# Performance work log

Hardware: AMD Instinct MI355X
Metric: run time of the kernel (lower is better)

The kernel has to match this reference:

```python
import jax, jax.numpy as jnp
import numpy as np

T = 8192  # number of points; covariance is T x T


def _rbf_cov(T_, lengthscale, variance):
    # Vectorized replacement of the O(T^2) python-loop kernel evaluation:
    # k(i, j) = variance * exp(-(i - j)^2 / (2 * lengthscale^2)) over integer grid.
    idx = jnp.arange(T_, dtype=jnp.float32)
    d = idx[:, None] - idx[None, :]                      # [T, T]
    return variance * jnp.exp(-(d * d) / (2.0 * lengthscale * lengthscale))


def setup_inputs() -> dict:
    key = jax.random.key(0)
    k1, = jax.random.split(key, 1)
    y = jax.random.normal(k1, (T,), dtype=jnp.float32)
    sigma_sq = jnp.ones((1,), dtype=jnp.float32)
    lengthscale = jnp.asarray(32.0, dtype=jnp.float32)
    variance = jnp.asarray(1.0, dtype=jnp.float32)
    return {"y": y, "sigma_sq": sigma_sq, "lengthscale": lengthscale, "variance": variance}


def reference(y, sigma_sq, lengthscale, variance):
    T_ = y.shape[0]
    K = _rbf_cov(T_, lengthscale, variance)              # [T, T]
    A = K + sigma_sq[0] * jnp.eye(T_, dtype=K.dtype)     # K + sigma^2 I
    yc = y.reshape(T_, 1)
    Ainv = jnp.linalg.inv(A)
    quad = yc.T @ Ainv @ yc                              # [1, 1]
    _, logdet = jnp.linalg.slogdet(A)
    return -0.5 * quad - 0.5 * logdet                    # [1, 1]
```

## Files before the change

### kernel.cpp

```cpp
#include <hip/hip_runtime.h>
#include <math.h>

#define T_PTS 8192
#define NSOLVE 64
#define NLOG   64
#define NBLK   (NSOLVE + NLOG + 1)
#define NTHR   512
#define NWAVE  (NTHR / 64)
#define NPT    128
#define PPT    10
#define WIN    (NPT * PPT)
#define CH     (T_PTS / NSOLVE)
#define HALO   ((WIN - CH) / 2)
#define BS     144
#define NGQ    3
#define NSTEP  3
#define GL     144
#define LDSN   1580
#define JH     256
#define BF     256
#define JB     (T_PTS / NLOG)
#define TQ     (BF / 4)
#define KCORR  768
#define MAGIC  0x13579BDFu

struct Slot { double q, l0, l1; unsigned int flag, pad; };

__device__ inline double blockReduceSum(double v, double* lds) {
#pragma unroll
    for (int o = 32; o > 0; o >>= 1) v += __shfl_down(v, o, 64);
    const int lane = threadIdx.x & 63, wid = threadIdx.x >> 6;
    __syncthreads();
    if (lane == 0) lds[wid] = v;
    __syncthreads();
    double r = 0.0;
    if (threadIdx.x == 0) {
#pragma unroll
        for (int i = 0; i < NWAVE; ++i) r += lds[i];
    }
    return r;
}

struct SolverSh {
    float dbuf[2][LDSN];
    float pac[3][PPT][NPT];
    float wAt[BS];
    float gt[BS];
    float hj[JH];
    float hpart[2][JH];
    float gpart[2][BS + 1];
    float gcen;
};
struct LogdetSh {
    float lgl[JB];
    float wlg[BF + 1];
    float pfj[4][JB];
};
union ShMem { SolverSh s; LogdetSh l; };

__global__ __launch_bounds__(NTHR, 1) void gp_mll_kernel(
    const float* __restrict__ y, const float* __restrict__ s2p,
    const float* __restrict__ ellp, const float* __restrict__ varp,
    float* __restrict__ out, unsigned char* __restrict__ wsb)
{
    __shared__ __align__(16) ShMem sh;
    __shared__ double redd[NWAVE];

    Slot*  slots = (Slot*)wsb;
    float* ckp   = (float*)(wsb + 4096);

    const int tid = threadIdx.x, bid = blockIdx.x;
    const float sig2 = s2p[0], ell = ellp[0], var = varp[0];
    const float inv2l2 = 1.0f / (2.0f * ell * ell);
    const float ang0 = 7.66990393942820614859e-4f;

    if (bid < NSOLVE) {
        SolverSh& S = sh.s;
        for (int d = tid; d < BS; d += NTHR)
            S.wAt[d] = var * expf(-(float)((d + 1) * (d + 1)) * inv2l2);
        for (int i = tid; i < LDSN; i += NTHR) { S.dbuf[0][i] = 0.f; S.dbuf[1][i] = 0.f; }
        __syncthreads();
        const float acen = sig2 + var;

        {
            const int jj = tid & 255, half = tid >> 8;
            float pf = (half == 0) ? acen : 0.f;
            for (int i = 0; i < BS / 2; ++i) {
                const int d = half * (BS / 2) + 1 + i;
                int m = (jj * d) & (T_PTS - 1);
                if (m >= T_PTS / 2) m -= T_PTS;
                pf += 2.f * S.wAt[d - 1] * __cosf(ang0 * (float)m);
            }
            S.hpart[half][jj] = pf;
        }
        __syncthreads();
        if (tid < JH) {
            const float fj = S.hpart[0][tid] + S.hpart[1][tid];
            S.hj[tid] = (fj - sig2) / fj;
        }
        __syncthreads();
        {
            const int d = tid & 255, jh = tid >> 8;
            if (d <= BS) {
                float pg = (jh == 0) ? S.hj[0] : 0.f;
                const int j0 = jh ? 128 : 1, j1 = jh ? 256 : 128;
                for (int j = j0; j < j1; ++j) {
                    int m = (j * d) & (T_PTS - 1);
                    if (m >= T_PTS / 2) m -= T_PTS;
                    pg += 2.f * S.hj[j] * __cosf(ang0 * (float)m);
                }
                S.gpart[jh][d] = pg;
            }
        }
        __syncthreads();
        if (tid <= BS) {
            const float hd = (S.gpart[0][tid] + S.gpart[1][tid]) * (1.0f / (float)T_PTS);
            if (tid == 0) S.gcen = (1.f - hd) / sig2;
            else          S.gt[tid - 1] = -hd / sig2;
        }

        const int pt = tid & (NPT - 1);
        const int q  = tid >> 7;
        const int i0 = pt * PPT;
        const int g0 = bid * CH - HALO + i0;
        const int cb = GL + i0;

        float yy[PPT], xx[PPT];
        if (q == 0) {
#pragma unroll
            for (int p = 0; p < PPT; ++p) {
                const bool in = (unsigned)(g0 + p) < (unsigned)T_PTS;
                yy[p] = in ? y[g0 + p] : 0.f;
                xx[p] = 0.f;
                S.dbuf[0][cb + p] = yy[p];
            }
        } else {
#pragma unroll
            for (int p = 0; p < PPT; ++p) { yy[p] = 0.f; xx[p] = 0.f; }
        }
        __syncthreads();

        for (int st = 0; st < NSTEP; ++st) {
            const float* src = S.dbuf[st & 1];
            float*       dst = S.dbuf[(st + 1) & 1];
            const float2* s2 = (const float2*)src;
            const bool isG = (st & 1) == 0;
            const float2* tap2 = (const float2*)(isG ? S.gt : S.wAt);
            const float  cen  = isG ? S.gcen : acen;

            float dk[PPT], ac[PPT];
            if (q == 0) {
#pragma unroll
                for (int h = 0; h < PPT / 2; ++h) {
                    float2 t = s2[(cb >> 1) + h];
                    dk[2*h] = t.x; dk[2*h+1] = t.y;
                }
#pragma unroll
                for (int p = 0; p < PPT; ++p) ac[p] = cen * dk[p];
            } else {
#pragma unroll
                for (int p = 0; p < PPT; ++p) { dk[p] = 0.f; ac[p] = 0.f; }
            }

#pragma unroll
            for (int j = 0; j < NGQ; ++j) {
                const int g = q * NGQ + j;
                const int lb2 = (cb - 12 * g - 12) >> 1;
                const int rb2 = (cb + 12 * g) >> 1;
                float la[22], ra[22], wg[12];
#pragma unroll
                for (int h = 0; h < 11; ++h) {
                    float2 t = s2[lb2 + h];
                    la[2*h] = t.x; la[2*h+1] = t.y;
                }
#pragma unroll
                for (int h = 0; h < 11; ++h) {
                    float2 t = s2[rb2 + h];
                    ra[2*h] = t.x; ra[2*h+1] = t.y;
                }
#pragma unroll
                for (int h = 0; h < 6; ++h) {
                    float2 t = tap2[6 * g + h];
                    wg[2*h] = t.x; wg[2*h+1] = t.y;
                }
#pragma unroll
                for (int k = 0; k < 12; ++k)
#pragma unroll
                    for (int p = 0; p < PPT; ++p)
                        ac[p] = fmaf(wg[k], la[p + 11 - k] + ra[p + 1 + k], ac[p]);
            }

            if (q > 0) {
#pragma unroll
                for (int p = 0; p < PPT; ++p) S.pac[q - 1][p][pt] = ac[p];
            }
            __syncthreads();

            if (q == 0) {
                float dn[PPT];
#pragma unroll
                for (int p = 0; p < PPT; ++p) {
                    const float act = ac[p] + S.pac[0][p][pt] + S.pac[1][p][pt]
                                            + S.pac[2][p][pt];
                    float val;
                    if (st == 0)       { xx[p] = act;  val = act; }
                    else if (st & 1)   { val = yy[p] - act; }
                    else               { xx[p] += act; val = xx[p]; }
                    const bool in = (unsigned)(g0 + p) < (unsigned)T_PTS;
                    dn[p] = in ? val : 0.f;
                }
                if (st < NSTEP - 1) {
                    float2* d2 = (float2*)dst;
#pragma unroll
                    for (int h = 0; h < PPT / 2; ++h)
                        d2[(cb >> 1) + h] = make_float2(dn[2*h], dn[2*h+1]);
                }
            }
            __syncthreads();
        }

        double qd = 0.0;
        if (q == 0) {
#pragma unroll
            for (int p = 0; p < PPT; ++p) {
                const int iw = i0 + p;
                if (iw >= HALO && iw < HALO + CH)
                    qd += (double)yy[p] * (double)xx[p];
            }
        }
        const double qs = blockReduceSum(qd, redd);
        if (tid == 0) {
            Slot* s = &slots[bid];
            s->q = qs; s->l0 = 0.0; s->l1 = 0.0;
            __threadfence();
            __hip_atomic_store(&s->flag, MAGIC, __ATOMIC_RELEASE, __HIP_MEMORY_SCOPE_AGENT);
        }
    } else if (bid < NSOLVE + NLOG) {
        LogdetSh& L = sh.l;
        const int lbk = bid - NSOLVE;
        for (int d = tid; d <= BF; d += NTHR)
            L.wlg[d] = var * expf(-(float)(d * d) * inv2l2);
        __syncthreads();

        const int jsub = tid & (JB - 1);
        const int qt   = tid >> 7;
        const int j    = lbk * JB + jsub;
        {
            float pf = 0.f;
            for (int i = 0; i < TQ; ++i) {
                const int d = qt * TQ + 1 + i;
                int m = (j * d) & (T_PTS - 1);
                if (m >= T_PTS / 2) m -= T_PTS;
                pf += 2.f * L.wlg[d] * __cosf(ang0 * (float)m);
            }
            L.pfj[qt][jsub] = pf;
        }
        __syncthreads();
        float lgj = 0.f;
        if (qt == 0) {
            const float fj = sig2 + var + L.pfj[0][jsub] + L.pfj[1][jsub]
                                        + L.pfj[2][jsub] + L.pfj[3][jsub];
            lgj = logf(fj);
            L.lgl[jsub] = lgj;
        }
        const double ls = blockReduceSum((double)lgj, redd);

        const int jbase = lbk * JB;
        const int k1 = tid + 1, k2 = tid + 513;
        float p1 = 0.f, p2 = 0.f;
        for (int jl = 0; jl < JB; ++jl) {
            const float lv = L.lgl[jl];
            const int jj = jbase + jl;
            int m1 = (jj * k1) & (T_PTS - 1);
            if (m1 >= T_PTS / 2) m1 -= T_PTS;
            p1 += lv * __cosf(ang0 * (float)m1);
            if (tid < 256) {
                int m2 = (jj * k2) & (T_PTS - 1);
                if (m2 >= T_PTS / 2) m2 -= T_PTS;
                p2 += lv * __cosf(ang0 * (float)m2);
            }
        }
        float* myck = ckp + lbk * KCORR;
        myck[tid] = p1;
        if (tid < 256) myck[512 + tid] = p2;
        __threadfence();
        __syncthreads();
        if (tid == 0) {
            Slot* s = &slots[bid];
            s->q = 0.0; s->l0 = ls; s->l1 = 0.0;
            __threadfence();
            __hip_atomic_store(&s->flag, MAGIC, __ATOMIC_RELEASE, __HIP_MEMORY_SCOPE_AGENT);
        }
    } else {
        if (tid < NSOLVE + NLOG) {
            while (__hip_atomic_load(&slots[tid].flag, __ATOMIC_ACQUIRE,
                                     __HIP_MEMORY_SCOPE_AGENT) != MAGIC)
                __builtin_amdgcn_s_sleep(2);
        }
        __syncthreads();
        double vq = 0.0, v0 = 0.0;
        if (tid < NSOLVE + NLOG) {
            Slot& s = slots[tid];
            vq = s.q; v0 = s.l0;
        }
        vq = blockReduceSum(vq, redd);
        v0 = blockReduceSum(v0, redd);
        float c1 = 0.f, c2 = 0.f;
        for (int b = 0; b < NLOG; ++b) {
            c1 += ckp[b * KCORR + tid];
            if (tid < 256) c2 += ckp[b * KCORR + 512 + tid];
        }
        const double invT = 1.0 / (double)T_PTS;
        double corrl = (double)(tid + 1) * ((double)c1 * invT) * ((double)c1 * invT);
        if (tid < 256)
            corrl += (double)(tid + 513) * ((double)c2 * invT) * ((double)c2 * invT);
        const double corr = blockReduceSum(corrl, redd);
        if (tid == 0)
            out[0] = (float)(-0.5 * vq - 0.5 * (v0 + corr));
    }
}

extern "C" void kernel_launch(void* const* d_in, const int* in_sizes, int n_in,
                              void* d_out, int out_size, void* d_ws, size_t ws_size,
                              hipStream_t stream) {
    const float* y    = (const float*)d_in[0];
    const float* sig2 = (const float*)d_in[1];
    const float* ell  = (const float*)d_in[2];
    const float* var  = (const float*)d_in[3];
    float* out = (float*)d_out;
    unsigned char* ws = (unsigned char*)d_ws;

    gp_mll_kernel<<<dim3(NBLK), dim3(NTHR), 0, stream>>>(y, sig2, ell, var, out, ws);
}
```

Before: 101.6 us.

## Merge logdet blocks into solve blocks to halve the block count

Each solve block now also runs one logdet chunk after its quadratic-form reduction, instead of using 64 separate logdet blocks. The grid shrinks from 129 to 65 blocks, and the final reducer polls 64 slots with a longer sleep between polls. This serialises the two phases inside each block, so per-block latency grows, in exchange for fewer blocks and less flag and slot traffic. On a GPU with many CUs, 129 blocks already fit concurrently, so the merge mainly lengthens the critical path.

```diff
diff --git a/kernel.cpp b/kernel.cpp
--- a/kernel.cpp
+++ b/kernel.cpp
@@ -3,8 +3,7 @@
 
 #define T_PTS 8192
 #define NSOLVE 64
-#define NLOG   64
-#define NBLK   (NSOLVE + NLOG + 1)
+#define NBLK   (NSOLVE + 1)
 #define NTHR   512
 #define NWAVE  (NTHR / 64)
 #define NPT    128
@@ -19,7 +18,7 @@
 #define LDSN   1580
 #define JH     256
 #define BF     256
-#define JB     (T_PTS / NLOG)
+#define JB     (T_PTS / NSOLVE)
 #define TQ     (BF / 4)
 #define KCORR  768
 #define MAGIC  0x13579BDFu
@@ -229,22 +228,17 @@
             }
         }
         const double qs = blockReduceSum(qd, redd);
-        if (tid == 0) {
-            Slot* s = &slots[bid];
-            s->q = qs; s->l0 = 0.0; s->l1 = 0.0;
-            __threadfence();
-            __hip_atomic_store(&s->flag, MAGIC, __ATOMIC_RELEASE, __HIP_MEMORY_SCOPE_AGENT);
-        }
-    } else if (bid < NSOLVE + NLOG) {
+        if (tid == 0) slots[bid].q = qs;
+
+        __syncthreads();
         LogdetSh& L = sh.l;
-        const int lbk = bid - NSOLVE;
         for (int d = tid; d <= BF; d += NTHR)
             L.wlg[d] = var * expf(-(float)(d * d) * inv2l2);
         __syncthreads();
 
         const int jsub = tid & (JB - 1);
         const int qt   = tid >> 7;
-        const int j    = lbk * JB + jsub;
+        const int j    = bid * JB + jsub;
         {
             float pf = 0.f;
             for (int i = 0; i < TQ; ++i) {
@@ -265,7 +259,7 @@
         }
         const double ls = blockReduceSum((double)lgj, redd);
 
-        const int jbase = lbk * JB;
+        const int jbase = bid * JB;
         const int k1 = tid + 1, k2 = tid + 513;
         float p1 = 0.f, p2 = 0.f;
         for (int jl = 0; jl < JB; ++jl) {
@@ -280,33 +274,31 @@
                 p2 += lv * __cosf(ang0 * (float)m2);
             }
         }
-        float* myck = ckp + lbk * KCORR;
+        float* myck = ckp + bid * KCORR;
         myck[tid] = p1;
         if (tid < 256) myck[512 + tid] = p2;
+        if (tid == 0) slots[bid].l0 = ls;
         __threadfence();
         __syncthreads();
-        if (tid == 0) {
-            Slot* s = &slots[bid];
-            s->q = 0.0; s->l0 = ls; s->l1 = 0.0;
-            __threadfence();
-            __hip_atomic_store(&s->flag, MAGIC, __ATOMIC_RELEASE, __HIP_MEMORY_SCOPE_AGENT);
-        }
+        if (tid == 0)
+            __hip_atomic_store(&slots[bid].flag, MAGIC, __ATOMIC_RELEASE,
+                               __HIP_MEMORY_SCOPE_AGENT);
     } else {
-        if (tid < NSOLVE + NLOG) {
+        if (tid < NSOLVE) {
             while (__hip_atomic_load(&slots[tid].flag, __ATOMIC_ACQUIRE,
                                      __HIP_MEMORY_SCOPE_AGENT) != MAGIC)
-                __builtin_amdgcn_s_sleep(2);
+                __builtin_amdgcn_s_sleep(16);
         }
         __syncthreads();
         double vq = 0.0, v0 = 0.0;
-        if (tid < NSOLVE + NLOG) {
+        if (tid < NSOLVE) {
             Slot& s = slots[tid];
             vq = s.q; v0 = s.l0;
         }
         vq = blockReduceSum(vq, redd);
         v0 = blockReduceSum(v0, redd);
         float c1 = 0.f, c2 = 0.f;
-        for (int b = 0; b < NLOG; ++b) {
+        for (int b = 0; b < NSOLVE; ++b) {
             c1 += ckp[b * KCORR + tid];
             if (tid < 256) c2 += ckp[b * KCORR + 512 + tid];
         }
```

Measured after the change: 120.0 us. +18.1%, slower.
